# Kernel optimization log

Hardware: AMD Instinct MI355X
Metric: run time of the kernel (lower is better)

Reference implementation:

```python
import jax, jax.numpy as jnp
import numpy as np

TAU = 2.0  # temperature_fn(step) constant


def setup_inputs() -> dict:
    key = jax.random.key(0)
    k_in, k_pad, k_g, k_w, k_cb = jax.random.split(key, 5)
    B, T, Din = 4, 4096, 1024
    G, V, D = 4, 1024, 128
    inputs = jax.random.normal(k_in, (B, T, Din), dtype=jnp.float32)
    paddings = jax.random.randint(k_pad, (B, T), 0, 2, dtype=jnp.int32)
    gumbel = jax.random.gumbel(k_g, (B, T, G, V), dtype=jnp.float32)
    W = jax.random.normal(k_w, (Din, G * V), dtype=jnp.float32) / np.sqrt(Din)
    b = jnp.zeros((G * V,), dtype=jnp.float32)
    codebook = jax.random.normal(k_cb, (G, V, D), dtype=jnp.float32)
    return {"inputs": inputs, "paddings": paddings, "gumbel": gumbel,
            "W": W, "b": b, "codebook": codebook}


def reference(inputs, paddings, gumbel, W, b, codebook):
    B, T, _ = inputs.shape
    G, V, D = codebook.shape
    # linear projection -> (B, T, G, V)
    logits = (inputs @ W + b).reshape(B, T, G, V)
    # training path: gumbel perturbation + temperature
    logits = (logits + gumbel) / TAU
    ids = jnp.argmax(logits, axis=-1)                      # (B, T, G)
    pad = paddings[..., None]                              # (B, T, 1)
    ids = jnp.where(pad.astype(bool), -1, ids)
    probs = jax.nn.softmax(logits, axis=-1)                # (B, T, G, V)
    nonpad = (1 - pad)[..., None].astype(logits.dtype)     # (B, T, 1, 1)
    probs = probs * nonpad
    onehots = jax.nn.one_hot(jnp.clip(ids, 0), V, dtype=logits.dtype)
    # straight-through estimator
    onehots = probs + jax.lax.stop_gradient(onehots - probs)
    # combine with codebook: quantized[b,t,g,d] = sum_v onehot[b,t,g,v] * codebook[g,v,d]
    quantized = jnp.einsum('btgv,gvd->btgd', onehots, codebook)
    quantized = quantized * nonpad
    quantized_flat = quantized.reshape(B, T, G * D)
    return ids, quantized_flat, probs
```

## Files before the change

### kernel.cpp

```cpp
#include <hip/hip_runtime.h>
#include <math.h>

constexpr int Mr = 16384;
constexpr int Nn = 4096;
constexpr int Kk = 1024;
constexpr int Gg = 4;
constexpr int Vv = 1024;
constexpr int Dd = 128;

typedef __attribute__((ext_vector_type(8))) short bf16x8;
typedef __attribute__((ext_vector_type(8))) unsigned short ushort8x;
typedef __attribute__((ext_vector_type(4))) float f32x4;

__device__ inline ushort f32_to_bf16(float x) {
    unsigned u = __float_as_uint(x);
    u += 0x7FFFu + ((u >> 16) & 1u);
    return (ushort)(u >> 16);
}

__device__ inline void gload16(const void* g, void* lds) {
    __builtin_amdgcn_global_load_lds(
        (const __attribute__((address_space(1))) unsigned int*)g,
        (__attribute__((address_space(3))) unsigned int*)lds, 16, 0, 0);
}

__global__ __launch_bounds__(256) void convert_a(
    const float* __restrict__ A, ushort* __restrict__ Abf)
{
    const size_t i = ((size_t)blockIdx.x * 256 + threadIdx.x) * 8;
    const float4 v0 = *(const float4*)(A + i);
    const float4 v1 = *(const float4*)(A + i + 4);
    ushort8x h;
    h[0] = f32_to_bf16(v0.x); h[1] = f32_to_bf16(v0.y);
    h[2] = f32_to_bf16(v0.z); h[3] = f32_to_bf16(v0.w);
    h[4] = f32_to_bf16(v1.x); h[5] = f32_to_bf16(v1.y);
    h[6] = f32_to_bf16(v1.z); h[7] = f32_to_bf16(v1.w);
    *(ushort8x*)(Abf + i) = h;
}

__global__ __launch_bounds__(256) void convert_wt(
    const float* __restrict__ W, ushort* __restrict__ Wt)
{
    __shared__ ushort t[64][80];
    const int n0 = blockIdx.x * 64;
    const int k0 = blockIdx.y * 64;
    const int tid = threadIdx.x;

    const int kl = tid >> 2;
    const int nl = (tid & 3) * 16;
    const float* src = W + (size_t)(k0 + kl) * Nn + n0 + nl;
#pragma unroll
    for (int j = 0; j < 16; j += 4) {
        const float4 v = *(const float4*)(src + j);
        t[nl + j + 0][kl] = f32_to_bf16(v.x);
        t[nl + j + 1][kl] = f32_to_bf16(v.y);
        t[nl + j + 2][kl] = f32_to_bf16(v.z);
        t[nl + j + 3][kl] = f32_to_bf16(v.w);
    }
    __syncthreads();
    const int nr = tid >> 2;
    const int kc = (tid & 3) * 16;
    ushort* dst = Wt + (size_t)(n0 + nr) * Kk + k0 + kc;
    *(ushort8x*)(dst)     = *(const ushort8x*)&t[nr][kc];
    *(ushort8x*)(dst + 8) = *(const ushort8x*)&t[nr][kc + 8];
}

__global__ __launch_bounds__(256, 2) void gemm_bf16(
    const ushort* __restrict__ Abf,
    const ushort* __restrict__ Bt,
    const float* __restrict__ bvec,
    float* __restrict__ C)
{
    __shared__ ushort Ah[128 * 64];
    __shared__ ushort Bh[128 * 64];

    const int tid  = threadIdx.x;
    const int lane = tid & 63;
    const int w    = tid >> 6;
    const int wm   = w >> 1;
    const int wn   = w & 1;
    const int quad = lane >> 4;
    const int l16  = lane & 15;

    const int bid = blockIdx.x;
    const int j   = bid >> 3;
    const int n_t = ((bid & 7) << 2) + (j & 3);
    const int m_t = j >> 2;
    const int m0  = m_t << 7;
    const int n0  = n_t << 7;

    const int srow = tid >> 3;
    const int scol = ((tid & 7) ^ (srow & 7)) << 3;
    const ushort* pa = Abf + (size_t)(m0 + srow) * Kk + scol;
    const ushort* pb = Bt  + (size_t)(n0 + srow) * Kk + scol;

    const int xr = (l16 & 7) << 3;

    f32x4 acc[4][4];
#pragma unroll
    for (int i = 0; i < 4; i++)
#pragma unroll
        for (int jj = 0; jj < 4; jj++) acc[i][jj] = (f32x4)(0.0f);

    for (int k0 = 0; k0 < Kk; k0 += 64) {
#pragma unroll
        for (int it = 0; it < 4; ++it)
            gload16(pa + (size_t)it * 32 * Kk + k0, &Ah[it * 2048 + w * 512]);
#pragma unroll
        for (int it = 0; it < 4; ++it)
            gload16(pb + (size_t)it * 32 * Kk + k0, &Bh[it * 2048 + w * 512]);
        __syncthreads();

#pragma unroll
        for (int kh = 0; kh < 2; ++kh) {
            bf16x8 af[4], bfr[4];
#pragma unroll
            for (int mi = 0; mi < 4; ++mi) {
                const int r = wm * 64 + mi * 16 + l16;
                af[mi] = *(const bf16x8*)&Ah[r * 64 + ((kh * 32 + quad * 8) ^ xr)];
            }
#pragma unroll
            for (int ni = 0; ni < 4; ++ni) {
                const int r = wn * 64 + ni * 16 + l16;
                bfr[ni] = *(const bf16x8*)&Bh[r * 64 + ((kh * 32 + quad * 8) ^ xr)];
            }
#pragma unroll
            for (int mi = 0; mi < 4; ++mi)
#pragma unroll
                for (int ni = 0; ni < 4; ++ni)
                    acc[mi][ni] = __builtin_amdgcn_mfma_f32_16x16x32_bf16(
                        af[mi], bfr[ni], acc[mi][ni], 0, 0, 0);
        }
        __syncthreads();
    }

    float bb[4];
#pragma unroll
    for (int ni = 0; ni < 4; ni++)
        bb[ni] = bvec[n0 + wn * 64 + ni * 16 + l16];
#pragma unroll
    for (int mi = 0; mi < 4; mi++) {
        const int mbase = m0 + wm * 64 + mi * 16 + quad * 4;
#pragma unroll
        for (int ni = 0; ni < 4; ni++) {
            const int n = n0 + wn * 64 + ni * 16 + l16;
            float* cp = C + (size_t)mbase * Nn + n;
#pragma unroll
            for (int r = 0; r < 4; r++)
                cp[(size_t)r * Nn] = acc[mi][ni][r] + bb[ni];
        }
    }
}

__global__ __launch_bounds__(256) void vq_epilogue(
    float* __restrict__ logits,
    const float* __restrict__ gumbel,
    const int* __restrict__ paddings,
    const float* __restrict__ A,
    const float* __restrict__ Wm,
    const float* __restrict__ bvec,
    const float* __restrict__ codebook,
    float* __restrict__ ids_out,
    float* __restrict__ quant_out)
{
    const int idx = blockIdx.x;
    const int m   = idx >> 2;
    const int g   = idx & 3;
    const int tid = threadIdx.x;
    const int w    = tid >> 6;
    const int lane = tid & 63;
    float* row = logits + (size_t)idx * Vv;

    if (paddings[m] != 0) {
        *(float4*)(row + tid * 4) = float4{0.f, 0.f, 0.f, 0.f};
        if (tid == 0) ids_out[idx] = -1.0f;
        if (tid < 32) *(float4*)(quant_out + (size_t)idx * Dd + tid * 4) = float4{0.f, 0.f, 0.f, 0.f};
        return;
    }

    const float* grow = gumbel + (size_t)idx * Vv;
    const float4 lr = *(const float4*)(row + tid * 4);
    const float4 gr = *(const float4*)(grow + tid * 4);
    float lv[4] = {(lr.x + gr.x) * 0.5f, (lr.y + gr.y) * 0.5f,
                   (lr.z + gr.z) * 0.5f, (lr.w + gr.w) * 0.5f};

    float bv1 = -1e30f, bv2 = -1e30f;
    int   bi1 = 0;
#pragma unroll
    for (int jj = 0; jj < 4; jj++) {
        const int v = tid * 4 + jj;
        if (lv[jj] > bv1) { bv2 = bv1; bv1 = lv[jj]; bi1 = v; }
        else if (lv[jj] > bv2) bv2 = lv[jj];
    }

#pragma unroll
    for (int off = 1; off < 64; off <<= 1) {
        const float ov1 = __shfl_xor(bv1, off);
        const float ov2 = __shfl_xor(bv2, off);
        const int   oi1 = __shfl_xor(bi1, off);
        if (ov1 > bv1 || (ov1 == bv1 && oi1 < bi1)) {
            bv2 = fmaxf(bv1, ov2); bv1 = ov1; bi1 = oi1;
        } else {
            bv2 = fmaxf(bv2, ov1);
        }
    }

    __shared__ float  sv1[4], sv2[4], ssum[4];
    __shared__ int    si1[4];
    __shared__ int    s_cnt;
    __shared__ int    s_cand[32];
    __shared__ double sdv[4];

    if (lane == 0) { sv1[w] = bv1; sv2[w] = bv2; si1[w] = bi1; }
    __syncthreads();

    float gv1 = sv1[0], gv2 = sv2[0];
    int   gi1 = si1[0];
#pragma unroll
    for (int ww = 1; ww < 4; ww++) {
        const float ov1 = sv1[ww], ov2 = sv2[ww];
        const int   oi  = si1[ww];
        if (ov1 > gv1 || (ov1 == gv1 && oi < gi1)) {
            gv2 = fmaxf(gv1, ov2); gv1 = ov1; gi1 = oi;
        } else {
            gv2 = fmaxf(gv2, ov1);
        }
    }
    const float gmax = gv1;
    const float gap  = gv1 - gv2;
    int id = gi1;

    const float MARGIN = 0.02f;
    if (gap < MARGIN) {
        if (tid == 0) s_cnt = 0;
        __syncthreads();
#pragma unroll
        for (int jj = 0; jj < 4; jj++) {
            if (lv[jj] >= gmax - MARGIN) {
                const int p = atomicAdd(&s_cnt, 1);
                if (p < 32) s_cand[p] = tid * 4 + jj;
            }
        }
        __syncthreads();
        const int ncand = min(s_cnt, 32);
        double bdv = -1e300;
        int    bdi = 1 << 30;
        const float* arow = A + (size_t)m * Kk;
        const float4 av = *(const float4*)(arow + tid * 4);
        for (int c = 0; c < ncand; ++c) {
            const int v = s_cand[c];
            const float* wcol = Wm + (g << 10) + v;
            const size_t kb = (size_t)tid * 4;
            double part = (double)av.x * (double)wcol[(kb + 0) * Nn]
                        + (double)av.y * (double)wcol[(kb + 1) * Nn]
                        + (double)av.z * (double)wcol[(kb + 2) * Nn]
                        + (double)av.w * (double)wcol[(kb + 3) * Nn];
#pragma unroll
            for (int off = 1; off < 64; off <<= 1)
                part += __shfl_xor(part, off);
            if (lane == 0) sdv[w] = part;
            __syncthreads();
            const double dot = sdv[0] + sdv[1] + sdv[2] + sdv[3]
                             + (double)bvec[(g << 10) + v];
            const double val = (dot + (double)grow[v]) * 0.5;
            if (val > bdv || (val == bdv && v < bdi)) { bdv = val; bdi = v; }
            __syncthreads();
        }
        id = bdi;
    }

    float ev[4];
    float se = 0.f;
#pragma unroll
    for (int jj = 0; jj < 4; jj++) { ev[jj] = __expf(lv[jj] - gmax); se += ev[jj]; }
#pragma unroll
    for (int off = 1; off < 64; off <<= 1)
        se += __shfl_xor(se, off);
    if (lane == 0) ssum[w] = se;
    __syncthreads();
    const float inv = 1.0f / (ssum[0] + ssum[1] + ssum[2] + ssum[3]);
    *(float4*)(row + tid * 4) = float4{ev[0] * inv, ev[1] * inv, ev[2] * inv, ev[3] * inv};

    if (tid == 0) ids_out[idx] = (float)id;
    if (tid < 32)
        *(float4*)(quant_out + (size_t)idx * Dd + tid * 4) =
            *(const float4*)(codebook + (size_t)(((g << 10) + id) << 7) + tid * 4);
}

extern "C" void kernel_launch(void* const* d_in, const int* in_sizes, int n_in,
                              void* d_out, int out_size, void* d_ws, size_t ws_size,
                              hipStream_t stream) {
    const float* inputs   = (const float*)d_in[0];
    const int*   paddings = (const int*)d_in[1];
    const float* gumbel   = (const float*)d_in[2];
    const float* W        = (const float*)d_in[3];
    const float* bvec     = (const float*)d_in[4];
    const float* codebook = (const float*)d_in[5];

    float* out       = (float*)d_out;
    float* ids_out   = out;
    float* quant_out = out + (size_t)Mr * Gg;
    float* probs_out = out + (size_t)Mr * Gg + (size_t)Mr * Gg * Dd;

    ushort* Abf = (ushort*)quant_out;
    ushort* Wt  = (ushort*)d_ws;

    convert_a<<<(Mr * Kk) / (256 * 8), 256, 0, stream>>>(inputs, Abf);
    convert_wt<<<dim3(Nn / 64, Kk / 64), 256, 0, stream>>>(W, Wt);

    gemm_bf16<<<(Mr / 128) * (Nn / 128), 256, 0, stream>>>(Abf, Wt, bvec, probs_out);

    vq_epilogue<<<Mr * Gg, 256, 0, stream>>>(probs_out, gumbel, paddings,
                                             inputs, W, bvec, codebook,
                                             ids_out, quant_out);
}
```

Measured before the change: 697.4 us.

## Rewrite GEMM as 256x256 tile with triple-buffered async LDS pipeline

Replaces the 128x128 bf16 GEMM with a 256x256 tile using 512 threads, K-step 32, and a three-slot LDS ring. Global-to-LDS loads for tile t+2 are issued while tile t is computed, with explicit vmcnt waits, split barriers and setprio around the MFMA bursts. It also changes the XCD-aware block mapping and the LDS swizzle. The aim is to hide global latency and raise reuse per byte loaded, at the cost of higher register and LDS use, which may lower occupancy.

```diff
diff --git a/kernel.cpp b/kernel.cpp
--- a/kernel.cpp
+++ b/kernel.cpp
@@ -65,73 +65,127 @@
     *(ushort8x*)(dst + 8) = *(const ushort8x*)&t[nr][kc + 8];
 }
 
-__global__ __launch_bounds__(256, 2) void gemm_bf16(
+constexpr int NT = Kk / 32;
+
+__global__ __launch_bounds__(512, 2) void gemm_bf16_256(
     const ushort* __restrict__ Abf,
     const ushort* __restrict__ Bt,
     const float* __restrict__ bvec,
     float* __restrict__ C)
 {
-    __shared__ ushort Ah[128 * 64];
-    __shared__ ushort Bh[128 * 64];
+    __shared__ ushort lds[3 * 16384];
 
     const int tid  = threadIdx.x;
     const int lane = tid & 63;
     const int w    = tid >> 6;
-    const int wm   = w >> 1;
-    const int wn   = w & 1;
+    const int wm   = w >> 2;
+    const int wn   = w & 3;
     const int quad = lane >> 4;
     const int l16  = lane & 15;
 
     const int bid = blockIdx.x;
-    const int j   = bid >> 3;
-    const int n_t = ((bid & 7) << 2) + (j & 3);
-    const int m_t = j >> 2;
-    const int m0  = m_t << 7;
-    const int n0  = n_t << 7;
-
-    const int srow = tid >> 3;
-    const int scol = ((tid & 7) ^ (srow & 7)) << 3;
-    const ushort* pa = Abf + (size_t)(m0 + srow) * Kk + scol;
-    const ushort* pb = Bt  + (size_t)(n0 + srow) * Kk + scol;
-
-    const int xr = (l16 & 7) << 3;
-
-    f32x4 acc[4][4];
-#pragma unroll
-    for (int i = 0; i < 4; i++)
-#pragma unroll
-        for (int jj = 0; jj < 4; jj++) acc[i][jj] = (f32x4)(0.0f);
-
-    for (int k0 = 0; k0 < Kk; k0 += 64) {
-#pragma unroll
-        for (int it = 0; it < 4; ++it)
-            gload16(pa + (size_t)it * 32 * Kk + k0, &Ah[it * 2048 + w * 512]);
-#pragma unroll
-        for (int it = 0; it < 4; ++it)
-            gload16(pb + (size_t)it * 32 * Kk + k0, &Bh[it * 2048 + w * 512]);
-        __syncthreads();
-
-#pragma unroll
-        for (int kh = 0; kh < 2; ++kh) {
-            bf16x8 af[4], bfr[4];
-#pragma unroll
-            for (int mi = 0; mi < 4; ++mi) {
-                const int r = wm * 64 + mi * 16 + l16;
-                af[mi] = *(const bf16x8*)&Ah[r * 64 + ((kh * 32 + quad * 8) ^ xr)];
-            }
-#pragma unroll
-            for (int ni = 0; ni < 4; ++ni) {
-                const int r = wn * 64 + ni * 16 + l16;
-                bfr[ni] = *(const bf16x8*)&Bh[r * 64 + ((kh * 32 + quad * 8) ^ xr)];
-            }
-#pragma unroll
-            for (int mi = 0; mi < 4; ++mi)
-#pragma unroll
-                for (int ni = 0; ni < 4; ++ni)
-                    acc[mi][ni] = __builtin_amdgcn_mfma_f32_16x16x32_bf16(
-                        af[mi], bfr[ni], acc[mi][ni], 0, 0, 0);
-        }
-        __syncthreads();
+    const int xcd = bid & 7;
+    const int idx = bid >> 3;
+    const int n_t = xcd * 2 + (idx >> 6);
+    const int m_t = idx & 63;
+    const int m0  = m_t << 8;
+    const int n0  = n_t << 8;
+
+    const int srow = tid >> 2;
+    const int sch  = (tid & 3) ^ ((srow >> 1) & 3);
+    const ushort* pa = Abf + (size_t)(m0 + srow) * Kk + sch * 8;
+    const ushort* pb = Bt  + (size_t)(n0 + srow) * Kk + sch * 8;
+    const int dst_w = w << 9;
+
+    int offB[4], offA0[4], offA1[4];
+#pragma unroll
+    for (int ni = 0; ni < 4; ++ni) {
+        const int r = wn * 64 + ni * 16 + l16;
+        offB[ni] = r * 32 + ((quad ^ ((r >> 1) & 3)) << 3);
+    }
+#pragma unroll
+    for (int mi = 0; mi < 4; ++mi) {
+        const int r0 = wm * 128 + mi * 16 + l16;
+        offA0[mi] = r0 * 32 + ((quad ^ ((r0 >> 1) & 3)) << 3);
+        const int r1 = r0 + 64;
+        offA1[mi] = r1 * 32 + ((quad ^ ((r1 >> 1) & 3)) << 3);
+    }
+
+    f32x4 acc[8][4];
+#pragma unroll
+    for (int i = 0; i < 8; i++)
+#pragma unroll
+        for (int j = 0; j < 4; j++) acc[i][j] = (f32x4)(0.0f);
+
+#pragma unroll
+    for (int tt = 0; tt < 2; ++tt) {
+        gload16(pa + (size_t)(0) * Kk + tt * 32,   &lds[tt * 16384 + 0    + dst_w]);
+        gload16(pa + (size_t)(128) * Kk + tt * 32, &lds[tt * 16384 + 4096 + dst_w]);
+        gload16(pb + (size_t)(0) * Kk + tt * 32,   &lds[tt * 16384 + 8192 + dst_w]);
+        gload16(pb + (size_t)(128) * Kk + tt * 32, &lds[tt * 16384 + 12288 + dst_w]);
+    }
+
+    int slot = 0;
+#pragma unroll 1
+    for (int t = 0; t < NT; ++t) {
+        const int snext = (slot + 2 >= 3) ? slot - 1 : slot + 2;
+        const ushort* As = &lds[slot * 16384];
+        const ushort* Bs = &lds[slot * 16384 + 8192];
+
+        if (t + 2 < NT) {
+            gload16(pa + (size_t)(0) * Kk + (t + 2) * 32,
+                    &lds[snext * 16384 + 0 + dst_w]);
+            gload16(pa + (size_t)(128) * Kk + (t + 2) * 32,
+                    &lds[snext * 16384 + 4096 + dst_w]);
+            asm volatile("s_waitcnt vmcnt(6)" ::: "memory");
+        } else if (t + 1 < NT) {
+            asm volatile("s_waitcnt vmcnt(4)" ::: "memory");
+        } else {
+            asm volatile("s_waitcnt vmcnt(0)" ::: "memory");
+        }
+        __builtin_amdgcn_sched_barrier(0);
+        __builtin_amdgcn_s_barrier();
+        __builtin_amdgcn_sched_barrier(0);
+
+        bf16x8 bfr[4], afr[4];
+#pragma unroll
+        for (int ni = 0; ni < 4; ++ni) bfr[ni] = *(const bf16x8*)&Bs[offB[ni]];
+#pragma unroll
+        for (int mi = 0; mi < 4; ++mi) afr[mi] = *(const bf16x8*)&As[offA0[mi]];
+        asm volatile("s_waitcnt lgkmcnt(0)" ::: "memory");
+        __builtin_amdgcn_sched_barrier(0);
+        __builtin_amdgcn_s_setprio(1);
+#pragma unroll
+        for (int mi = 0; mi < 4; ++mi)
+#pragma unroll
+            for (int ni = 0; ni < 4; ++ni)
+                acc[mi][ni] = __builtin_amdgcn_mfma_f32_16x16x32_bf16(
+                    afr[mi], bfr[ni], acc[mi][ni], 0, 0, 0);
+        __builtin_amdgcn_s_setprio(0);
+
+        if (t + 2 < NT) {
+            gload16(pb + (size_t)(0) * Kk + (t + 2) * 32,
+                    &lds[snext * 16384 + 8192 + dst_w]);
+            gload16(pb + (size_t)(128) * Kk + (t + 2) * 32,
+                    &lds[snext * 16384 + 12288 + dst_w]);
+        }
+        bf16x8 afr2[4];
+#pragma unroll
+        for (int mi = 0; mi < 4; ++mi) afr2[mi] = *(const bf16x8*)&As[offA1[mi]];
+        asm volatile("s_waitcnt lgkmcnt(0)" ::: "memory");
+        __builtin_amdgcn_sched_barrier(0);
+        __builtin_amdgcn_s_setprio(1);
+#pragma unroll
+        for (int mi = 0; mi < 4; ++mi)
+#pragma unroll
+            for (int ni = 0; ni < 4; ++ni)
+                acc[mi + 4][ni] = __builtin_amdgcn_mfma_f32_16x16x32_bf16(
+                    afr2[mi], bfr[ni], acc[mi + 4][ni], 0, 0, 0);
+        __builtin_amdgcn_s_setprio(0);
+        __builtin_amdgcn_s_barrier();
+        __builtin_amdgcn_sched_barrier(0);
+
+        slot = (slot + 1 >= 3) ? 0 : slot + 1;
     }
 
     float bb[4];
@@ -139,8 +193,8 @@
     for (int ni = 0; ni < 4; ni++)
         bb[ni] = bvec[n0 + wn * 64 + ni * 16 + l16];
 #pragma unroll
-    for (int mi = 0; mi < 4; mi++) {
-        const int mbase = m0 + wm * 64 + mi * 16 + quad * 4;
+    for (int mi = 0; mi < 8; mi++) {
+        const int mbase = m0 + wm * 128 + mi * 16 + quad * 4;
 #pragma unroll
         for (int ni = 0; ni < 4; ni++) {
             const int n = n0 + wn * 64 + ni * 16 + l16;
@@ -308,7 +362,7 @@
     convert_a<<<(Mr * Kk) / (256 * 8), 256, 0, stream>>>(inputs, Abf);
     convert_wt<<<dim3(Nn / 64, Kk / 64), 256, 0, stream>>>(W, Wt);
 
-    gemm_bf16<<<(Mr / 128) * (Nn / 128), 256, 0, stream>>>(Abf, Wt, bvec, probs_out);
+    gemm_bf16_256<<<(Mr / 256) * (Nn / 256), 512, 0, stream>>>(Abf, Wt, bvec, probs_out);
 
     vq_epilogue<<<Mr * Gg, 256, 0, stream>>>(probs_out, gumbel, paddings,
                                              inputs, W, bvec, codebook,
```

New measurement: 707.3 us. No clear change (+1.4%).

## Compact non-padded rows and skip GEMM work for padded timesteps

Applied to the files above, without the earlier changes.

A single-block prefix-scan kernel builds a map of non-padded rows and their count. The bf16 conversion of the inputs then packs only those rows into a dense buffer. The GEMM returns early for tiles beyond the compacted row count and scatters its results back to the original row positions. Padded rows end with zeroed probs and quantized values anyway, so their logits are not needed, which removes roughly the padded fraction of GEMM and conversion work. In exchange it adds a serial single-block scan, an indirect row scatter in the GEMM epilogue, and it relies on the epilogue kernel never reading logits for padded rows.

```diff
diff --git a/kernel.cpp b/kernel.cpp
--- a/kernel.cpp
+++ b/kernel.cpp
@@ -24,18 +24,51 @@
         (__attribute__((address_space(3))) unsigned int*)lds, 16, 0, 0);
 }
 
-__global__ __launch_bounds__(256) void convert_a(
-    const float* __restrict__ A, ushort* __restrict__ Abf)
-{
-    const size_t i = ((size_t)blockIdx.x * 256 + threadIdx.x) * 8;
-    const float4 v0 = *(const float4*)(A + i);
-    const float4 v1 = *(const float4*)(A + i + 4);
-    ushort8x h;
-    h[0] = f32_to_bf16(v0.x); h[1] = f32_to_bf16(v0.y);
-    h[2] = f32_to_bf16(v0.z); h[3] = f32_to_bf16(v0.w);
-    h[4] = f32_to_bf16(v1.x); h[5] = f32_to_bf16(v1.y);
-    h[6] = f32_to_bf16(v1.z); h[7] = f32_to_bf16(v1.w);
-    *(ushort8x*)(Abf + i) = h;
+__global__ __launch_bounds__(256) void compact_rows(
+    const int* __restrict__ paddings, int* __restrict__ cmap,
+    int* __restrict__ mp)
+{
+    const int t = threadIdx.x;
+    __shared__ int s[256];
+    int c = 0;
+#pragma unroll 4
+    for (int k = 0; k < 64; ++k) c += (paddings[k * 256 + t] == 0);
+    s[t] = c;
+    __syncthreads();
+    for (int d = 1; d < 256; d <<= 1) {
+        const int v = (t >= d) ? s[t - d] : 0;
+        __syncthreads();
+        s[t] += v;
+        __syncthreads();
+    }
+    int pos = s[t] - c;
+    for (int k = 0; k < 64; ++k) {
+        const int m = k * 256 + t;
+        if (paddings[m] == 0) cmap[pos++] = m;
+    }
+    if (t == 255) mp[0] = s[255];
+}
+
+__global__ __launch_bounds__(256) void convert_a_compact(
+    const float* __restrict__ A, const int* __restrict__ cmap,
+    const int* __restrict__ mp, ushort* __restrict__ Abf)
+{
+    const int Mp  = mp[0];
+    const int Mpr = (Mp + 127) & ~127;
+    const int j   = blockIdx.x * 2 + (threadIdx.x >> 7);
+    if (j >= Mpr) return;
+    const int col = (threadIdx.x & 127) * 8;
+    ushort8x h = (ushort8x)0;
+    if (j < Mp) {
+        const float* src = A + (size_t)cmap[j] * Kk + col;
+        const float4 v0 = *(const float4*)(src);
+        const float4 v1 = *(const float4*)(src + 4);
+        h[0] = f32_to_bf16(v0.x); h[1] = f32_to_bf16(v0.y);
+        h[2] = f32_to_bf16(v0.z); h[3] = f32_to_bf16(v0.w);
+        h[4] = f32_to_bf16(v1.x); h[5] = f32_to_bf16(v1.y);
+        h[6] = f32_to_bf16(v1.z); h[7] = f32_to_bf16(v1.w);
+    }
+    *(ushort8x*)(Abf + (size_t)j * Kk + col) = h;
 }
 
 __global__ __launch_bounds__(256) void convert_wt(
@@ -69,6 +102,8 @@
     const ushort* __restrict__ Abf,
     const ushort* __restrict__ Bt,
     const float* __restrict__ bvec,
+    const int* __restrict__ cmap,
+    const int* __restrict__ mp,
     float* __restrict__ C)
 {
     __shared__ ushort Ah[128 * 64];
@@ -89,6 +124,9 @@
     const int m0  = m_t << 7;
     const int n0  = n_t << 7;
 
+    const int Mp = mp[0];
+    if (m0 >= ((Mp + 127) & ~127)) return;
+
     const int srow = tid >> 3;
     const int scol = ((tid & 7) ^ (srow & 7)) << 3;
     const ushort* pa = Abf + (size_t)(m0 + srow) * Kk + scol;
@@ -140,14 +178,17 @@
         bb[ni] = bvec[n0 + wn * 64 + ni * 16 + l16];
 #pragma unroll
     for (int mi = 0; mi < 4; mi++) {
-        const int mbase = m0 + wm * 64 + mi * 16 + quad * 4;
+        const int j0 = m0 + wm * 64 + mi * 16 + quad * 4;
+        if (j0 >= Mp) continue;
+        const int4 cm = *(const int4*)&cmap[j0];
+        const int cr[4] = {cm.x, cm.y, cm.z, cm.w};
 #pragma unroll
         for (int ni = 0; ni < 4; ni++) {
             const int n = n0 + wn * 64 + ni * 16 + l16;
-            float* cp = C + (size_t)mbase * Nn + n;
 #pragma unroll
             for (int r = 0; r < 4; r++)
-                cp[(size_t)r * Nn] = acc[mi][ni][r] + bb[ni];
+                if (j0 + r < Mp)
+                    C[(size_t)cr[r] * Nn + n] = acc[mi][ni][r] + bb[ni];
         }
     }
 }
@@ -302,13 +343,17 @@
     float* quant_out = out + (size_t)Mr * Gg;
     float* probs_out = out + (size_t)Mr * Gg + (size_t)Mr * Gg * Dd;
 
-    ushort* Abf = (ushort*)quant_out;
-    ushort* Wt  = (ushort*)d_ws;
-
-    convert_a<<<(Mr * Kk) / (256 * 8), 256, 0, stream>>>(inputs, Abf);
+    int*    cmap = (int*)ids_out;
+    int*    mp   = cmap + Mr;
+    ushort* Abf  = (ushort*)quant_out;
+    ushort* Wt   = (ushort*)d_ws;
+
+    compact_rows<<<1, 256, 0, stream>>>(paddings, cmap, mp);
+    convert_a_compact<<<Mr / 2, 256, 0, stream>>>(inputs, cmap, mp, Abf);
     convert_wt<<<dim3(Nn / 64, Kk / 64), 256, 0, stream>>>(W, Wt);
 
-    gemm_bf16<<<(Mr / 128) * (Nn / 128), 256, 0, stream>>>(Abf, Wt, bvec, probs_out);
+    gemm_bf16<<<(Mr / 128) * (Nn / 128), 256, 0, stream>>>(Abf, Wt, bvec,
+                                                           cmap, mp, probs_out);
 
     vq_epilogue<<<Mr * Gg, 256, 0, stream>>>(probs_out, gumbel, paddings,
                                              inputs, W, bvec, codebook,
```

Measured after the change: 625.0 us. 1.12x faster.
